# Kernel optimization log

Hardware: AMD Instinct MI355X
Metric: run time of the kernel (lower is better)

Reference implementation:

```python
import jax, jax.numpy as jnp
import numpy as np

N_NODES, N_EDGES, N_GRAPHS = 50000, 600000, 64
SEQ_DIM, HID = 384, 128


def setup_inputs() -> dict:
    key = jax.random.key(0)
    ks = jax.random.split(key, 12)
    inp = {}
    inp["seq_emb"] = jax.random.normal(ks[0], (N_GRAPHS, SEQ_DIM), jnp.float32)
    inp["node_x"] = jax.random.normal(ks[1], (N_NODES, SEQ_DIM), jnp.float32)
    inp["edge_index"] = jax.random.randint(ks[2], (2, N_EDGES), 0, N_NODES, dtype=jnp.int32)
    inp["node_batch"] = jnp.sort(jax.random.randint(ks[3], (N_NODES,), 0, N_GRAPHS, dtype=jnp.int32))
    # learned parameters (fan-in scaled)
    inp["W1"] = jax.random.normal(ks[4], (SEQ_DIM, HID), jnp.float32) / np.sqrt(SEQ_DIM)
    inp["b1"] = jnp.zeros((HID,), jnp.float32)
    inp["W2"] = jax.random.normal(ks[5], (HID, HID), jnp.float32) / np.sqrt(HID)
    inp["b2"] = jnp.zeros((HID,), jnp.float32)
    inp["Wf"] = jax.random.normal(ks[6], (SEQ_DIM + HID, 128), jnp.float32) / np.sqrt(SEQ_DIM + HID)
    inp["bf"] = jnp.zeros((128,), jnp.float32)
    inp["Wtp"] = jax.random.normal(ks[7], (128, 2), jnp.float32) / np.sqrt(128)
    inp["btp"] = jnp.zeros((2,), jnp.float32)
    inp["Wp"] = jax.random.normal(ks[8], (128, 1), jnp.float32) / np.sqrt(128)
    inp["bp"] = jnp.zeros((1,), jnp.float32)
    return inp


def _gcn_conv(x, W, b, src, dst, norm, n_nodes):
    # PyG GCNConv: out = A_hat @ (x W) + b, A_hat = D^-1/2 (A+I) D^-1/2
    h = x @ W                                   # [N, H]
    msg = h[src] * norm[:, None]                # [E+N, H] gather + scale
    return jax.ops.segment_sum(msg, dst, num_segments=n_nodes) + b


def reference(seq_emb, node_x, edge_index, node_batch,
              W1, b1, W2, b2, Wf, bf, Wtp, btp, Wp, bp):
    n = node_x.shape[0]
    b_graphs = seq_emb.shape[0]
    loops = jnp.arange(n, dtype=edge_index.dtype)
    src = jnp.concatenate([edge_index[0], loops])
    dst = jnp.concatenate([edge_index[1], loops])
    # symmetric normalization with self-loops (deg >= 1)
    deg = jax.ops.segment_sum(jnp.ones_like(dst, dtype=node_x.dtype), dst, num_segments=n)
    dinv = deg ** -0.5
    norm = dinv[src] * dinv[dst]

    g = jax.nn.relu(_gcn_conv(node_x, W1, b1, src, dst, norm, n))
    g = jax.nn.relu(_gcn_conv(g, W2, b2, src, dst, norm, n))

    # global mean pool over graphs
    sums = jax.ops.segment_sum(g, node_batch, num_segments=b_graphs)
    cnts = jax.ops.segment_sum(jnp.ones((n,), g.dtype), node_batch, num_segments=b_graphs)
    pooled = sums / jnp.maximum(cnts, 1.0)[:, None]

    fused = jax.nn.relu(jnp.concatenate([seq_emb, pooled], axis=1) @ Wf + bf)
    tp_logits = fused @ Wtp + btp
    prom_pred = fused @ Wp + bp
    return (tp_logits, prom_pred)
```

## Files before the change

### kernel.cpp

```cpp
#include <hip/hip_runtime.h>


#define HID 128

typedef __attribute__((ext_vector_type(8))) short bf16x8;
typedef __attribute__((ext_vector_type(4))) short bf16x4;
typedef __attribute__((ext_vector_type(4))) float f32x4;

static __device__ __forceinline__ short f2bf(float f) {
  union { float f; unsigned u; } v; v.f = f;
  unsigned r = v.u + 0x7fff + ((v.u >> 16) & 1);
  return (short)(r >> 16);
}
static __device__ __forceinline__ float bf2f(short s) {
  union { unsigned u; float f; } v;
  v.u = ((unsigned)(unsigned short)s) << 16;
  return v.f;
}

__global__ __launch_bounds__(256) void prep_w_k(const float* __restrict__ W1,
                                                short* __restrict__ W1t,
                                                const float* __restrict__ W2,
                                                short* __restrict__ W2t,
                                                int* __restrict__ deg, int N) {
  int idx = blockIdx.x * 256 + threadIdx.x;
  if (idx < 384 * HID) {
    int k = idx >> 7;
    int c = idx & 127;
    W1t[(size_t)c * 384 + k] = f2bf(W1[idx]);
  } else if (idx < 384 * HID + HID * HID) {
    int j = idx - 384 * HID;
    int k = j >> 7;
    int c = j & 127;
    W2t[(size_t)c * HID + k] = f2bf(W2[j]);
  }
  if (idx < N) deg[idx] = 0;
}

__global__ __launch_bounds__(256) void hist_k(const int* __restrict__ dst,
                                              int* __restrict__ cnt, int E) {
  int i = blockIdx.x * 256 + threadIdx.x;
  if (i < E) atomicAdd(&cnt[dst[i]], 1);
}

__global__ __launch_bounds__(256) void scan_bsum(const int* __restrict__ cnt,
                                                 int* __restrict__ bsum,
                                                 float* __restrict__ dinv, int n) {
  __shared__ int sm[256];
  int i = blockIdx.x * 256 + threadIdx.x;
  int v = (i < n) ? cnt[i] : 0;
  if (i < n) dinv[i] = rsqrtf((float)(v + 1));
  sm[threadIdx.x] = v;
  __syncthreads();
  for (int off = 128; off > 0; off >>= 1) {
    if (threadIdx.x < off) sm[threadIdx.x] += sm[threadIdx.x + off];
    __syncthreads();
  }
  if (threadIdx.x == 0) bsum[blockIdx.x] = sm[0];
}

__global__ __launch_bounds__(256) void scan_offsets(const int* __restrict__ cnt,
                                                    const int* __restrict__ bsum,
                                                    int* __restrict__ offs,
                                                    int* __restrict__ cur,
                                                    float* __restrict__ sums,
                                                    int nsum, int n, int nb) {
  __shared__ int sm[256];
  int t = threadIdx.x;
  int bid = blockIdx.x;
  int zi = bid * 256 + t;
  if (zi < nsum) sums[zi] = 0.f;
  int bv = (t < nb) ? bsum[t] : 0;
  sm[t] = bv;
  __syncthreads();
  for (int off = 1; off < 256; off <<= 1) {
    int add = (t >= off) ? sm[t - off] : 0;
    __syncthreads();
    sm[t] += add;
    __syncthreads();
  }
  int base = (bid > 0) ? sm[bid - 1] : 0;
  __syncthreads();
  int i = bid * 256 + t;
  int v = (i < n) ? cnt[i] : 0;
  sm[t] = v;
  __syncthreads();
  for (int off = 1; off < 256; off <<= 1) {
    int add = (t >= off) ? sm[t - off] : 0;
    __syncthreads();
    sm[t] += add;
    __syncthreads();
  }
  if (i < n) {
    offs[i] = base + sm[t] - v;
    cur[i] = 0;
  }
  if (i == n - 1) offs[n] = base + sm[t];
}

__global__ __launch_bounds__(256) void fill_k(const int* __restrict__ src,
                                              const int* __restrict__ dst,
                                              const int* __restrict__ offs,
                                              int* __restrict__ cur,
                                              int* __restrict__ csr, int E) {
  int i = blockIdx.x * 256 + threadIdx.x;
  if (i >= E) return;
  int d = dst[i];
  int p = offs[d] + atomicAdd(&cur[d], 1);
  csr[p] = src[i];
}

__global__ __launch_bounds__(256) void mfma_gemm1_k(const float* __restrict__ Af,
                                                    const short* __restrict__ Wt,
                                                    const float* __restrict__ scale,
                                                    short* __restrict__ C, int M) {
  constexpr int K = 384;
  constexpr int BK = 64;
  constexpr int ROWE = BK + 8;
  __shared__ short As[64 * ROWE];
  __shared__ short Bs[128 * ROWE];
  __shared__ float dln[64];

  const int tid = threadIdx.x;
  const int wave = tid >> 6;
  const int lane = tid & 63;
  const int l15 = lane & 15;
  const int lk = lane >> 4;
  const int mh = (wave >> 1) * 32;
  const int nh = (wave & 1) * 64;
  const int row0 = blockIdx.x * 64;

  if (tid < 64) {
    int r = row0 + tid;
    dln[tid] = (r < M) ? scale[r] : 0.f;
  }

  f32x4 acc[2][4] = {};

  for (int k0 = 0; k0 < K; k0 += BK) {
    __syncthreads();
#pragma unroll
    for (int it = 0; it < 4; ++it) {
      int f = tid + it * 256;
      int r = f >> 4;
      int kc = (f & 15) << 2;
      int gr = row0 + r;
      float4 v = make_float4(0.f, 0.f, 0.f, 0.f);
      if (gr < M) v = *(const float4*)&Af[(size_t)gr * K + k0 + kc];
      bf16x4 s;
      s[0] = f2bf(v.x); s[1] = f2bf(v.y); s[2] = f2bf(v.z); s[3] = f2bf(v.w);
      *(bf16x4*)&As[r * ROWE + kc] = s;
    }
#pragma unroll
    for (int it = 0; it < 4; ++it) {
      int f = tid + it * 256;
      int r = f >> 3;
      int kc = (f & 7) << 3;
      *(bf16x8*)&Bs[r * ROWE + kc] =
          *(const bf16x8*)&Wt[(size_t)r * K + k0 + kc];
    }
    __syncthreads();
#pragma unroll
    for (int ks = 0; ks < 2; ++ks) {
      bf16x8 af[2], bfr[4];
#pragma unroll
      for (int mf = 0; mf < 2; ++mf)
        af[mf] = *(const bf16x8*)&As[(mh + mf * 16 + l15) * ROWE + ks * 32 + lk * 8];
#pragma unroll
      for (int nf = 0; nf < 4; ++nf)
        bfr[nf] = *(const bf16x8*)&Bs[(nh + nf * 16 + l15) * ROWE + ks * 32 + lk * 8];
#pragma unroll
      for (int mf = 0; mf < 2; ++mf)
#pragma unroll
        for (int nf = 0; nf < 4; ++nf)
          acc[mf][nf] = __builtin_amdgcn_mfma_f32_16x16x32_bf16(
              af[mf], bfr[nf], acc[mf][nf], 0, 0, 0);
    }
  }
#pragma unroll
  for (int mf = 0; mf < 2; ++mf) {
#pragma unroll
    for (int r = 0; r < 4; ++r) {
      int lr = mh + mf * 16 + lk * 4 + r;
      int gr = row0 + lr;
      if (gr >= M) continue;
      float s = dln[lr];
#pragma unroll
      for (int nf = 0; nf < 4; ++nf)
        C[(size_t)gr * HID + nh + nf * 16 + l15] = f2bf(acc[mf][nf][r] * s);
    }
  }
}

__global__ __launch_bounds__(256) void gemm2_agg_k(const short* __restrict__ Hs,
                                                   const int* __restrict__ offs,
                                                   const int* __restrict__ csr,
                                                   const float* __restrict__ dinv,
                                                   const float* __restrict__ b1,
                                                   const short* __restrict__ Wt,
                                                   short* __restrict__ C, int M) {
  constexpr int K = 128;
  constexpr int BK = 64;
  constexpr int ROWE = BK + 8;
  __shared__ short As[64 * ROWE];
  __shared__ short Bs[128 * ROWE];
  __shared__ float dln[64];

  const int tid = threadIdx.x;
  const int wave = tid >> 6;
  const int lane = tid & 63;
  const int l15 = lane & 15;
  const int lk = lane >> 4;
  const int mh = (wave >> 1) * 32;
  const int nh = (wave & 1) * 64;
  const int row0 = blockIdx.x * 64;

  if (tid < 64) {
    int r = row0 + tid;
    dln[tid] = (r < M) ? dinv[r] : 0.f;
  }

  const int srow = tid >> 2;
  const int sl = tid & 3;
  const int gr = row0 + srow;
  const bool valid = gr < M;
  int es = 0, ee = 0;
  float dvv = 0.f;
  if (valid) {
    es = offs[gr];
    ee = offs[gr + 1];
    dvv = dinv[gr];
  }

  f32x4 acc[2][4] = {};

  for (int k0 = 0; k0 < K; k0 += BK) {
    __syncthreads();
#pragma unroll
    for (int it = 0; it < 4; ++it) {
      int f = tid + it * 256;
      int r = f >> 3;
      int kc = (f & 7) << 3;
      *(bf16x8*)&Bs[r * ROWE + kc] =
          *(const bf16x8*)&Wt[(size_t)r * K + k0 + kc];
    }
    {
      const int cb = k0 + sl * 16;
      float a[16];
#pragma unroll
      for (int q = 0; q < 16; ++q) a[q] = 0.f;
      if (valid) {
        const short* rs = &Hs[(size_t)gr * HID + cb];
        bf16x8 s0 = *(const bf16x8*)rs;
        bf16x8 s1 = *(const bf16x8*)(rs + 8);
#pragma unroll
        for (int q = 0; q < 8; ++q) { a[q] = bf2f(s0[q]); a[8 + q] = bf2f(s1[q]); }
        int p = es;
        for (; p + 4 <= ee; p += 4) {
          int u0 = csr[p + 0];
          int u1 = csr[p + 1];
          int u2 = csr[p + 2];
          int u3 = csr[p + 3];
          const short* r0 = &Hs[(size_t)u0 * HID + cb];
          const short* r1 = &Hs[(size_t)u1 * HID + cb];
          const short* r2 = &Hs[(size_t)u2 * HID + cb];
          const short* r3 = &Hs[(size_t)u3 * HID + cb];
          bf16x8 x0a = *(const bf16x8*)r0, x0b = *(const bf16x8*)(r0 + 8);
          bf16x8 x1a = *(const bf16x8*)r1, x1b = *(const bf16x8*)(r1 + 8);
          bf16x8 x2a = *(const bf16x8*)r2, x2b = *(const bf16x8*)(r2 + 8);
          bf16x8 x3a = *(const bf16x8*)r3, x3b = *(const bf16x8*)(r3 + 8);
#pragma unroll
          for (int q = 0; q < 8; ++q) {
            a[q]     += (bf2f(x0a[q]) + bf2f(x1a[q])) + (bf2f(x2a[q]) + bf2f(x3a[q]));
            a[8 + q] += (bf2f(x0b[q]) + bf2f(x1b[q])) + (bf2f(x2b[q]) + bf2f(x3b[q]));
          }
        }
        for (; p < ee; ++p) {
          int u = csr[p];
          const short* r0 = &Hs[(size_t)u * HID + cb];
          bf16x8 xa = *(const bf16x8*)r0, xb = *(const bf16x8*)(r0 + 8);
#pragma unroll
          for (int q = 0; q < 8; ++q) { a[q] += bf2f(xa[q]); a[8 + q] += bf2f(xb[q]); }
        }
        float4 bb0 = *(const float4*)&b1[cb];
        float4 bb1 = *(const float4*)&b1[cb + 4];
        float4 bb2 = *(const float4*)&b1[cb + 8];
        float4 bb3 = *(const float4*)&b1[cb + 12];
        float bbv[16] = {bb0.x, bb0.y, bb0.z, bb0.w, bb1.x, bb1.y, bb1.z, bb1.w,
                         bb2.x, bb2.y, bb2.z, bb2.w, bb3.x, bb3.y, bb3.z, bb3.w};
#pragma unroll
        for (int q = 0; q < 16; ++q)
          a[q] = fmaxf(fmaf(a[q], dvv, bbv[q]), 0.f);
      }
      bf16x8 o0, o1;
#pragma unroll
      for (int q = 0; q < 8; ++q) { o0[q] = f2bf(a[q]); o1[q] = f2bf(a[8 + q]); }
      *(bf16x8*)&As[srow * ROWE + sl * 16] = o0;
      *(bf16x8*)&As[srow * ROWE + sl * 16 + 8] = o1;
    }
    __syncthreads();
#pragma unroll
    for (int ks = 0; ks < 2; ++ks) {
      bf16x8 af[2], bfr[4];
#pragma unroll
      for (int mf = 0; mf < 2; ++mf)
        af[mf] = *(const bf16x8*)&As[(mh + mf * 16 + l15) * ROWE + ks * 32 + lk * 8];
#pragma unroll
      for (int nf = 0; nf < 4; ++nf)
        bfr[nf] = *(const bf16x8*)&Bs[(nh + nf * 16 + l15) * ROWE + ks * 32 + lk * 8];
#pragma unroll
      for (int mf = 0; mf < 2; ++mf)
#pragma unroll
        for (int nf = 0; nf < 4; ++nf)
          acc[mf][nf] = __builtin_amdgcn_mfma_f32_16x16x32_bf16(
              af[mf], bfr[nf], acc[mf][nf], 0, 0, 0);
    }
  }
#pragma unroll
  for (int mf = 0; mf < 2; ++mf) {
#pragma unroll
    for (int r = 0; r < 4; ++r) {
      int lr = mh + mf * 16 + lk * 4 + r;
      int g2 = row0 + lr;
      if (g2 >= M) continue;
      float s = dln[lr];
#pragma unroll
      for (int nf = 0; nf < 4; ++nf)
        C[(size_t)g2 * HID + nh + nf * 16 + l15] = f2bf(acc[mf][nf][r] * s);
    }
  }
}

__global__ __launch_bounds__(512) void agg2_pool_k(const short* __restrict__ Hs,
                                                   const int* __restrict__ offs,
                                                   const int* __restrict__ csr,
                                                   const float* __restrict__ dinv,
                                                   const float* __restrict__ b2,
                                                   const int* __restrict__ batch,
                                                   float* __restrict__ sums,
                                                   int N) {
  const int nid = threadIdx.x >> 3;
  const int l8 = threadIdx.x & 7;
  const int v = blockIdx.x * 64 + nid;
  const int cb = l8 * 16;
  float a[16];
#pragma unroll
  for (int q = 0; q < 16; ++q) a[q] = 0.f;
  const bool valid = v < N;
  if (valid) {
    int es = offs[v];
    int ee = offs[v + 1];
    const short* rs = &Hs[(size_t)v * HID + cb];
    bf16x8 s0 = *(const bf16x8*)rs;
    bf16x8 s1 = *(const bf16x8*)(rs + 8);
#pragma unroll
    for (int q = 0; q < 8; ++q) { a[q] = bf2f(s0[q]); a[8 + q] = bf2f(s1[q]); }
    int p = es;
    for (; p + 4 <= ee; p += 4) {
      int u0 = csr[p + 0];
      int u1 = csr[p + 1];
      int u2 = csr[p + 2];
      int u3 = csr[p + 3];
      const short* r0 = &Hs[(size_t)u0 * HID + cb];
      const short* r1 = &Hs[(size_t)u1 * HID + cb];
      const short* r2 = &Hs[(size_t)u2 * HID + cb];
      const short* r3 = &Hs[(size_t)u3 * HID + cb];
      bf16x8 x0a = *(const bf16x8*)r0, x0b = *(const bf16x8*)(r0 + 8);
      bf16x8 x1a = *(const bf16x8*)r1, x1b = *(const bf16x8*)(r1 + 8);
      bf16x8 x2a = *(const bf16x8*)r2, x2b = *(const bf16x8*)(r2 + 8);
      bf16x8 x3a = *(const bf16x8*)r3, x3b = *(const bf16x8*)(r3 + 8);
#pragma unroll
      for (int q = 0; q < 8; ++q) {
        a[q]     += (bf2f(x0a[q]) + bf2f(x1a[q])) + (bf2f(x2a[q]) + bf2f(x3a[q]));
        a[8 + q] += (bf2f(x0b[q]) + bf2f(x1b[q])) + (bf2f(x2b[q]) + bf2f(x3b[q]));
      }
    }
    for (; p < ee; ++p) {
      int u = csr[p];
      const short* r0 = &Hs[(size_t)u * HID + cb];
      bf16x8 xa = *(const bf16x8*)r0, xb = *(const bf16x8*)(r0 + 8);
#pragma unroll
      for (int q = 0; q < 8; ++q) { a[q] += bf2f(xa[q]); a[8 + q] += bf2f(xb[q]); }
    }
    float dv = dinv[v];
    float4 bb0 = *(const float4*)&b2[cb];
    float4 bb1 = *(const float4*)&b2[cb + 4];
    float4 bb2v = *(const float4*)&b2[cb + 8];
    float4 bb3 = *(const float4*)&b2[cb + 12];
    float bbv[16] = {bb0.x, bb0.y, bb0.z, bb0.w, bb1.x, bb1.y, bb1.z, bb1.w,
                     bb2v.x, bb2v.y, bb2v.z, bb2v.w, bb3.x, bb3.y, bb3.z, bb3.w};
#pragma unroll
    for (int q = 0; q < 16; ++q)
      a[q] = fmaxf(fmaf(a[q], dv, bbv[q]), 0.f);
  }
  __shared__ float ot[64 * 133];
  __shared__ int bsm[64];
#pragma unroll
  for (int q = 0; q < 16; ++q) ot[nid * 133 + cb + q] = a[q];
  if (threadIdx.x < 64) {
    int vv = blockIdx.x * 64 + threadIdx.x;
    bsm[threadIdx.x] = batch[vv < N ? vv : N - 1];
  }
  __syncthreads();
  int j = threadIdx.x & 127;
  int h = threadIdx.x >> 7;
  int r0 = h * 16;
  int g_cur = bsm[r0];
  float acc = 0.f;
#pragma unroll
  for (int rr = r0; rr < r0 + 16; ++rr) {
    int g = bsm[rr];
    if (g != g_cur) {
      atomicAdd(&sums[(size_t)g_cur * HID + j], acc);
      acc = 0.f;
      g_cur = g;
    }
    acc += ot[rr * 133 + j];
  }
  atomicAdd(&sums[(size_t)g_cur * HID + j], acc);
}

__global__ __launch_bounds__(128) void head_k(const float* __restrict__ seq,
                                              const float* __restrict__ sums,
                                              const int* __restrict__ batch,
                                              const float* __restrict__ Wf,
                                              const float* __restrict__ bf,
                                              const float* __restrict__ Wtp,
                                              const float* __restrict__ btp,
                                              const float* __restrict__ Wp,
                                              const float* __restrict__ bp,
                                              float* __restrict__ outp,
                                              int B, int SEQ, int n) {
  int g = blockIdx.x;
  int t = threadIdx.x;
  __shared__ float xin[512];
  __shared__ float fs[128];
  int lo = 0, hi = n;
  while (lo < hi) { int mid = (lo + hi) >> 1; if (batch[mid] < g) lo = mid + 1; else hi = mid; }
  int start = lo;
  hi = n;
  while (lo < hi) { int mid = (lo + hi) >> 1; if (batch[mid] <= g) lo = mid + 1; else hi = mid; }
  float inv_cnt = 1.f / fmaxf((float)(lo - start), 1.f);
  for (int i = t; i < SEQ; i += 128) xin[i] = seq[(size_t)g * SEQ + i];
  xin[SEQ + t] = sums[g * HID + t] * inv_cnt;
  __syncthreads();
  float acc = bf[t];
#pragma unroll 8
  for (int k = 0; k < 512; ++k) acc = fmaf(xin[k], Wf[(size_t)k * HID + t], acc);
  fs[t] = fmaxf(acc, 0.f);
  __syncthreads();
  if (t == 0) {
    float a0 = btp[0], a1 = btp[1], a2 = bp[0];
    for (int k = 0; k < 128; ++k) {
      float f = fs[k];
      a0 = fmaf(f, Wtp[k * 2 + 0], a0);
      a1 = fmaf(f, Wtp[k * 2 + 1], a1);
      a2 = fmaf(f, Wp[k], a2);
    }
    outp[g * 2 + 0] = a0;
    outp[g * 2 + 1] = a1;
    outp[B * 2 + g] = a2;
  }
}

extern "C" void kernel_launch(void* const* d_in, const int* in_sizes, int n_in,
                              void* d_out, int out_size, void* d_ws, size_t ws_size,
                              hipStream_t stream) {
  const float* seq_emb = (const float*)d_in[0];
  const float* node_x  = (const float*)d_in[1];
  const int*   eidx    = (const int*)d_in[2];
  const int*   nbatch  = (const int*)d_in[3];
  const float* W1  = (const float*)d_in[4];
  const float* b1  = (const float*)d_in[5];
  const float* W2  = (const float*)d_in[6];
  const float* b2  = (const float*)d_in[7];
  const float* Wf  = (const float*)d_in[8];
  const float* bfb = (const float*)d_in[9];
  const float* Wtp = (const float*)d_in[10];
  const float* btp = (const float*)d_in[11];
  const float* Wp  = (const float*)d_in[12];
  const float* bp  = (const float*)d_in[13];

  const int N = in_sizes[3];
  const int E = in_sizes[2] / 2;
  const int SEQ = 384;
  const int B = in_sizes[0] / SEQ;

  char* w = (char*)d_ws;
  auto alloc = [&](size_t bytes) -> void* {
    void* p = (void*)w;
    w += (bytes + 255) & ~(size_t)255;
    return p;
  };
  float* dinv   = (float*)alloc((size_t)N * 4);
  int*   deg    = (int*)alloc((size_t)N * 4);
  int*   cur    = (int*)alloc((size_t)N * 4);
  int*   offs   = (int*)alloc((size_t)(N + 1) * 4);
  int*   bsum   = (int*)alloc(1024);
  int*   csr    = (int*)alloc((size_t)E * 4);
  short* W1t    = (short*)alloc((size_t)SEQ * HID * 2);
  short* W2t    = (short*)alloc((size_t)HID * HID * 2);
  short* bufC   = (short*)alloc((size_t)N * HID * 2);
  short* bufD   = (short*)alloc((size_t)N * HID * 2);
  float* sums   = (float*)alloc((size_t)B * HID * 4);

  const int* srcp = eidx;
  const int* dstp = eidx + E;

  int gE = (E + 255) / 256;
  int gN = (N + 255) / 256;
  int wElems = SEQ * HID + HID * HID;
  int gP = (max(wElems, N) + 255) / 256;

  prep_w_k<<<gP, 256, 0, stream>>>(W1, W1t, W2, W2t, deg, N);
  hist_k<<<gE, 256, 0, stream>>>(dstp, deg, E);
  scan_bsum<<<gN, 256, 0, stream>>>(deg, bsum, dinv, N);
  scan_offsets<<<gN, 256, 0, stream>>>(deg, bsum, offs, cur, sums, B * HID, N, gN);
  fill_k<<<gE, 256, 0, stream>>>(srcp, dstp, offs, cur, csr, E);

  int gG = (N + 63) / 64;
  mfma_gemm1_k<<<gG, 256, 0, stream>>>(node_x, W1t, dinv, bufC, N);
  gemm2_agg_k<<<gG, 256, 0, stream>>>(bufC, offs, csr, dinv, b1, W2t, bufD, N);
  agg2_pool_k<<<gG, 512, 0, stream>>>(bufD, offs, csr, dinv, b2, nbatch, sums, N);
  head_k<<<B, 128, 0, stream>>>(seq_emb, sums, nbatch, Wf, bfb, Wtp, btp, Wp, bp,
                                (float*)d_out, B, SEQ, N);
}
```

Measured before the change: 194.3 us.

## Aggregate full rows once in gemm2 and deepen gather unrolling in agg2

In the fused layer-2 aggregate+GEMM kernel, the K loop over two 64-wide chunks is removed. Each thread now gathers 32 contiguous columns per neighbor in one pass and stages the full 128-wide A and W tiles in LDS. This walks the CSR adjacency once instead of twice and drops a barrier round, at the cost of more registers and a larger LDS footprint. The pooling aggregation kernel gains an 8-way unrolled gather for more loads in flight, and CSR index reads use nontemporal loads.

```diff
diff --git a/kernel.cpp b/kernel.cpp
--- a/kernel.cpp
+++ b/kernel.cpp
@@ -200,8 +200,7 @@
                                                    const short* __restrict__ Wt,
                                                    short* __restrict__ C, int M) {
   constexpr int K = 128;
-  constexpr int BK = 64;
-  constexpr int ROWE = BK + 8;
+  constexpr int ROWE = K + 8;
   __shared__ short As[64 * ROWE];
   __shared__ short Bs[128 * ROWE];
   __shared__ float dln[64];
@@ -220,101 +219,100 @@
     dln[tid] = (r < M) ? dinv[r] : 0.f;
   }
 
-  const int srow = tid >> 2;
-  const int sl = tid & 3;
-  const int gr = row0 + srow;
-  const bool valid = gr < M;
-  int es = 0, ee = 0;
-  float dvv = 0.f;
-  if (valid) {
-    es = offs[gr];
-    ee = offs[gr + 1];
-    dvv = dinv[gr];
-  }
+#pragma unroll
+  for (int it = 0; it < 8; ++it) {
+    int f = tid + it * 256;
+    int r = f >> 4;
+    int kc = (f & 15) << 3;
+    *(bf16x8*)&Bs[r * ROWE + kc] = *(const bf16x8*)&Wt[(size_t)r * K + kc];
+  }
+
+  {
+    const int srow = tid >> 2;
+    const int sl = tid & 3;
+    const int gr = row0 + srow;
+    const int cb = sl * 32;
+    float a[32];
+#pragma unroll
+    for (int q = 0; q < 32; ++q) a[q] = 0.f;
+    if (gr < M) {
+      int es = offs[gr];
+      int ee = offs[gr + 1];
+      float dvv = dinv[gr];
+      const short* rs = &Hs[(size_t)gr * HID + cb];
+#pragma unroll
+      for (int h = 0; h < 4; ++h) {
+        bf16x8 sv = *(const bf16x8*)(rs + h * 8);
+#pragma unroll
+        for (int q = 0; q < 8; ++q) a[h * 8 + q] = bf2f(sv[q]);
+      }
+      int p = es;
+      for (; p + 4 <= ee; p += 4) {
+        int u0 = __builtin_nontemporal_load(&csr[p + 0]);
+        int u1 = __builtin_nontemporal_load(&csr[p + 1]);
+        int u2 = __builtin_nontemporal_load(&csr[p + 2]);
+        int u3 = __builtin_nontemporal_load(&csr[p + 3]);
+        const short* r0 = &Hs[(size_t)u0 * HID + cb];
+        const short* r1 = &Hs[(size_t)u1 * HID + cb];
+        const short* r2 = &Hs[(size_t)u2 * HID + cb];
+        const short* r3 = &Hs[(size_t)u3 * HID + cb];
+#pragma unroll
+        for (int h = 0; h < 4; ++h) {
+          bf16x8 x0 = *(const bf16x8*)(r0 + h * 8);
+          bf16x8 x1 = *(const bf16x8*)(r1 + h * 8);
+          bf16x8 x2 = *(const bf16x8*)(r2 + h * 8);
+          bf16x8 x3 = *(const bf16x8*)(r3 + h * 8);
+#pragma unroll
+          for (int q = 0; q < 8; ++q)
+            a[h * 8 + q] += (bf2f(x0[q]) + bf2f(x1[q])) +
+                            (bf2f(x2[q]) + bf2f(x3[q]));
+        }
+      }
+      for (; p < ee; ++p) {
+        int u = __builtin_nontemporal_load(&csr[p]);
+        const short* r0 = &Hs[(size_t)u * HID + cb];
+#pragma unroll
+        for (int h = 0; h < 4; ++h) {
+          bf16x8 x = *(const bf16x8*)(r0 + h * 8);
+#pragma unroll
+          for (int q = 0; q < 8; ++q) a[h * 8 + q] += bf2f(x[q]);
+        }
+      }
+#pragma unroll
+      for (int h = 0; h < 8; ++h) {
+        float4 bb = *(const float4*)&b1[cb + h * 4];
+        a[h * 4 + 0] = fmaxf(fmaf(a[h * 4 + 0], dvv, bb.x), 0.f);
+        a[h * 4 + 1] = fmaxf(fmaf(a[h * 4 + 1], dvv, bb.y), 0.f);
+        a[h * 4 + 2] = fmaxf(fmaf(a[h * 4 + 2], dvv, bb.z), 0.f);
+        a[h * 4 + 3] = fmaxf(fmaf(a[h * 4 + 3], dvv, bb.w), 0.f);
+      }
+    }
+#pragma unroll
+    for (int h = 0; h < 4; ++h) {
+      bf16x8 o;
+#pragma unroll
+      for (int q = 0; q < 8; ++q) o[q] = f2bf(a[h * 8 + q]);
+      *(bf16x8*)&As[srow * ROWE + cb + h * 8] = o;
+    }
+  }
+  __syncthreads();
 
   f32x4 acc[2][4] = {};
-
-  for (int k0 = 0; k0 < K; k0 += BK) {
-    __syncthreads();
-#pragma unroll
-    for (int it = 0; it < 4; ++it) {
-      int f = tid + it * 256;
-      int r = f >> 3;
-      int kc = (f & 7) << 3;
-      *(bf16x8*)&Bs[r * ROWE + kc] =
-          *(const bf16x8*)&Wt[(size_t)r * K + k0 + kc];
-    }
-    {
-      const int cb = k0 + sl * 16;
-      float a[16];
-#pragma unroll
-      for (int q = 0; q < 16; ++q) a[q] = 0.f;
-      if (valid) {
-        const short* rs = &Hs[(size_t)gr * HID + cb];
-        bf16x8 s0 = *(const bf16x8*)rs;
-        bf16x8 s1 = *(const bf16x8*)(rs + 8);
-#pragma unroll
-        for (int q = 0; q < 8; ++q) { a[q] = bf2f(s0[q]); a[8 + q] = bf2f(s1[q]); }
-        int p = es;
-        for (; p + 4 <= ee; p += 4) {
-          int u0 = csr[p + 0];
-          int u1 = csr[p + 1];
-          int u2 = csr[p + 2];
-          int u3 = csr[p + 3];
-          const short* r0 = &Hs[(size_t)u0 * HID + cb];
-          const short* r1 = &Hs[(size_t)u1 * HID + cb];
-          const short* r2 = &Hs[(size_t)u2 * HID + cb];
-          const short* r3 = &Hs[(size_t)u3 * HID + cb];
-          bf16x8 x0a = *(const bf16x8*)r0, x0b = *(const bf16x8*)(r0 + 8);
-          bf16x8 x1a = *(const bf16x8*)r1, x1b = *(const bf16x8*)(r1 + 8);
-          bf16x8 x2a = *(const bf16x8*)r2, x2b = *(const bf16x8*)(r2 + 8);
-          bf16x8 x3a = *(const bf16x8*)r3, x3b = *(const bf16x8*)(r3 + 8);
-#pragma unroll
-          for (int q = 0; q < 8; ++q) {
-            a[q]     += (bf2f(x0a[q]) + bf2f(x1a[q])) + (bf2f(x2a[q]) + bf2f(x3a[q]));
-            a[8 + q] += (bf2f(x0b[q]) + bf2f(x1b[q])) + (bf2f(x2b[q]) + bf2f(x3b[q]));
-          }
-        }
-        for (; p < ee; ++p) {
-          int u = csr[p];
-          const short* r0 = &Hs[(size_t)u * HID + cb];
-          bf16x8 xa = *(const bf16x8*)r0, xb = *(const bf16x8*)(r0 + 8);
-#pragma unroll
-          for (int q = 0; q < 8; ++q) { a[q] += bf2f(xa[q]); a[8 + q] += bf2f(xb[q]); }
-        }
-        float4 bb0 = *(const float4*)&b1[cb];
-        float4 bb1 = *(const float4*)&b1[cb + 4];
-        float4 bb2 = *(const float4*)&b1[cb + 8];
-        float4 bb3 = *(const float4*)&b1[cb + 12];
-        float bbv[16] = {bb0.x, bb0.y, bb0.z, bb0.w, bb1.x, bb1.y, bb1.z, bb1.w,
-                         bb2.x, bb2.y, bb2.z, bb2.w, bb3.x, bb3.y, bb3.z, bb3.w};
-#pragma unroll
-        for (int q = 0; q < 16; ++q)
-          a[q] = fmaxf(fmaf(a[q], dvv, bbv[q]), 0.f);
-      }
-      bf16x8 o0, o1;
-#pragma unroll
-      for (int q = 0; q < 8; ++q) { o0[q] = f2bf(a[q]); o1[q] = f2bf(a[8 + q]); }
-      *(bf16x8*)&As[srow * ROWE + sl * 16] = o0;
-      *(bf16x8*)&As[srow * ROWE + sl * 16 + 8] = o1;
-    }
-    __syncthreads();
-#pragma unroll
-    for (int ks = 0; ks < 2; ++ks) {
-      bf16x8 af[2], bfr[4];
-#pragma unroll
-      for (int mf = 0; mf < 2; ++mf)
-        af[mf] = *(const bf16x8*)&As[(mh + mf * 16 + l15) * ROWE + ks * 32 + lk * 8];
+#pragma unroll
+  for (int ks = 0; ks < 4; ++ks) {
+    bf16x8 af[2], bfr[4];
+#pragma unroll
+    for (int mf = 0; mf < 2; ++mf)
+      af[mf] = *(const bf16x8*)&As[(mh + mf * 16 + l15) * ROWE + ks * 32 + lk * 8];
+#pragma unroll
+    for (int nf = 0; nf < 4; ++nf)
+      bfr[nf] = *(const bf16x8*)&Bs[(nh + nf * 16 + l15) * ROWE + ks * 32 + lk * 8];
+#pragma unroll
+    for (int mf = 0; mf < 2; ++mf)
 #pragma unroll
       for (int nf = 0; nf < 4; ++nf)
-        bfr[nf] = *(const bf16x8*)&Bs[(nh + nf * 16 + l15) * ROWE + ks * 32 + lk * 8];
-#pragma unroll
-      for (int mf = 0; mf < 2; ++mf)
-#pragma unroll
-        for (int nf = 0; nf < 4; ++nf)
-          acc[mf][nf] = __builtin_amdgcn_mfma_f32_16x16x32_bf16(
-              af[mf], bfr[nf], acc[mf][nf], 0, 0, 0);
-    }
+        acc[mf][nf] = __builtin_amdgcn_mfma_f32_16x16x32_bf16(
+            af[mf], bfr[nf], acc[mf][nf], 0, 0, 0);
   }
 #pragma unroll
   for (int mf = 0; mf < 2; ++mf) {
@@ -356,11 +354,30 @@
 #pragma unroll
     for (int q = 0; q < 8; ++q) { a[q] = bf2f(s0[q]); a[8 + q] = bf2f(s1[q]); }
     int p = es;
+    for (; p + 8 <= ee; p += 8) {
+      int u[8];
+#pragma unroll
+      for (int q = 0; q < 8; ++q) u[q] = __builtin_nontemporal_load(&csr[p + q]);
+      bf16x8 xa[8], xb[8];
+#pragma unroll
+      for (int q = 0; q < 8; ++q) {
+        const short* r0 = &Hs[(size_t)u[q] * HID + cb];
+        xa[q] = *(const bf16x8*)r0;
+        xb[q] = *(const bf16x8*)(r0 + 8);
+      }
+#pragma unroll
+      for (int q = 0; q < 8; ++q)
+#pragma unroll
+        for (int r = 0; r < 8; ++r) {
+          a[r] += bf2f(xa[q][r]);
+          a[8 + r] += bf2f(xb[q][r]);
+        }
+    }
     for (; p + 4 <= ee; p += 4) {
-      int u0 = csr[p + 0];
-      int u1 = csr[p + 1];
-      int u2 = csr[p + 2];
-      int u3 = csr[p + 3];
+      int u0 = __builtin_nontemporal_load(&csr[p + 0]);
+      int u1 = __builtin_nontemporal_load(&csr[p + 1]);
+      int u2 = __builtin_nontemporal_load(&csr[p + 2]);
+      int u3 = __builtin_nontemporal_load(&csr[p + 3]);
       const short* r0 = &Hs[(size_t)u0 * HID + cb];
       const short* r1 = &Hs[(size_t)u1 * HID + cb];
       const short* r2 = &Hs[(size_t)u2 * HID + cb];
@@ -376,7 +393,7 @@
       }
     }
     for (; p < ee; ++p) {
-      int u = csr[p];
+      int u = __builtin_nontemporal_load(&csr[p]);
       const short* r0 = &Hs[(size_t)u * HID + cb];
       bf16x8 xa = *(const bf16x8*)r0, xb = *(const bf16x8*)(r0 + 8);
 #pragma unroll
```

Result: slower. 210.1 us (+8.1%).
